# Optimization experiments

Measured on AMD Instinct MI355X. Metric: run time of the kernel, lower is better.

The kernel has to match this reference:

```python
import jax, jax.numpy as jnp
import numpy as np

EMBED = 512
MLP_DIM = 2048
B, T = 4, 4096
EPS = 1e-5


def setup_inputs() -> dict:
    key = jax.random.key(0)
    ks = jax.random.split(key, 8)
    s = lambda fan_in: 1.0 / np.sqrt(fan_in)
    inp = {
        "x": jax.random.normal(ks[0], (B, T, EMBED), dtype=jnp.float32),
        "Wq": jax.random.uniform(ks[1], (EMBED, EMBED), jnp.float32, -s(EMBED), s(EMBED)),
        "bq": jnp.zeros((EMBED,), jnp.float32),
        "Wk": jax.random.uniform(ks[2], (EMBED, EMBED), jnp.float32, -s(EMBED), s(EMBED)),
        "bk": jnp.zeros((EMBED,), jnp.float32),
        "Wv": jax.random.uniform(ks[3], (EMBED, EMBED), jnp.float32, -s(EMBED), s(EMBED)),
        "bv": jnp.zeros((EMBED,), jnp.float32),
        "W1": jax.random.uniform(ks[4], (EMBED, MLP_DIM), jnp.float32, -s(EMBED), s(EMBED)),
        "b1": jnp.zeros((MLP_DIM,), jnp.float32),
        "W2": jax.random.uniform(ks[5], (MLP_DIM, EMBED), jnp.float32, -s(MLP_DIM), s(MLP_DIM)),
        "b2": jnp.zeros((EMBED,), jnp.float32),
        "ln1_g": jnp.ones((EMBED,), jnp.float32),
        "ln1_b": jnp.zeros((EMBED,), jnp.float32),
        "ln2_g": jnp.ones((EMBED,), jnp.float32),
        "ln2_b": jnp.zeros((EMBED,), jnp.float32),
    }
    return inp


def _layernorm(x, g, b):
    mu = x.mean(-1, keepdims=True)
    var = ((x - mu) ** 2).mean(-1, keepdims=True)
    return (x - mu) * jax.lax.rsqrt(var + EPS) * g + b


def reference(x, Wq, bq, Wk, bk, Wv, bv, W1, b1, W2, b2, ln1_g, ln1_b, ln2_g, ln2_b):
    # pre-LN causal self-attention (single head)
    h = _layernorm(x, ln1_g, ln1_b)
    q = h @ Wq + bq  # [B,T,D]
    k = h @ Wk + bk
    v = h @ Wv + bv
    scale = 1.0 / jnp.sqrt(jnp.float32(EMBED))
    scores = jnp.einsum("btd,bsd->bts", q, k) * scale  # [B,T,T]
    mask = jnp.tril(jnp.ones((T, T), dtype=bool))
    scores = jnp.where(mask, scores, -jnp.inf)
    # NOTE: source applies softmax over the ENTIRE [T,T] matrix per batch
    # element (global max + global sum), not per-row. Replicate exactly.
    m = scores.max(axis=(-2, -1), keepdims=True)
    e = jnp.exp(scores - m)
    attn = e / e.sum(axis=(-2, -1), keepdims=True)
    x = x + jnp.einsum("bts,bsd->btd", attn, v)
    # MLP
    h2 = _layernorm(x, ln2_g, ln2_b)
    x = x + (jax.nn.gelu(h2 @ W1 + b1, approximate=False) @ W2 + b2)
    return x
```

## Files before the change

kernel.cpp:

```cpp
#include <hip/hip_runtime.h>
#include <hip/hip_bf16.h>
#include <math.h>

#define EMBED 512
#define MLPD  2048
#define NB    4
#define TS    4096
#define BT    (NB*TS)
#define BK    64
#define NTILES_TRI 528

typedef __attribute__((ext_vector_type(4))) float f32x4;
typedef __attribute__((ext_vector_type(8))) short s16x8;
typedef __hip_bfloat16 bf16_t;

__device__ __forceinline__ void gload16(const void* g, void* l) {
  __builtin_amdgcn_global_load_lds(
      (const __attribute__((address_space(1))) void*)g,
      (__attribute__((address_space(3))) void*)l, 16, 0, 0);
}

__device__ __forceinline__ float fast_erf(float y) {
  const float ay = fabsf(y);
  const float t = __builtin_amdgcn_rcpf(1.0f + 0.3275911f*ay);
  float poly = 1.061405429f;
  poly = poly*t - 1.453152027f;
  poly = poly*t + 1.421413741f;
  poly = poly*t - 0.284496736f;
  poly = poly*t + 0.254829592f;
  poly = poly*t;
  const float e = 1.0f - poly*__expf(-ay*ay);
  return copysignf(e, y);
}

__device__ __forceinline__ void gemm_core(
    const bf16_t* __restrict__ A, int lda,
    const bf16_t* __restrict__ Bt, int ldb,
    int kmax, bf16_t* Alds, bf16_t* Blds, f32x4 acc[4][4])
{
  const int tid = threadIdx.x;
  const int w  = tid >> 6;
  const int l  = tid & 63;
  const int wr = w >> 1, wc = w & 1;
  const int fr = l & 15, fg = l >> 4;

  #pragma unroll
  for (int i = 0; i < 4; ++i)
    #pragma unroll
    for (int j = 0; j < 4; ++j)
      #pragma unroll
      for (int e = 0; e < 4; ++e)
        acc[i][j][e] = 0.0f;

  const int srow = w*32 + (l >> 3);
  const int scol = (l & 7)*8;

  for (int k0 = 0; k0 < kmax; k0 += BK) {
    __syncthreads();
    #pragma unroll
    for (int c = 0; c < 4; ++c) {
      const bf16_t* ga = A  + (size_t)(srow + c*8)*lda + (k0 + scol);
      const bf16_t* gb = Bt + (size_t)(srow + c*8)*ldb + (k0 + scol);
      gload16(ga, Alds + (w*32 + c*8)*BK);
      gload16(gb, Blds + (w*32 + c*8)*BK);
    }
    __syncthreads();
    #pragma unroll
    for (int kk = 0; kk < BK; kk += 32) {
      s16x8 av[4], bv[4];
      #pragma unroll
      for (int mf = 0; mf < 4; ++mf)
        av[mf] = *(const s16x8*)(Alds + (wr*64 + mf*16 + fr)*BK + kk + fg*8);
      #pragma unroll
      for (int nf = 0; nf < 4; ++nf)
        bv[nf] = *(const s16x8*)(Blds + (wc*64 + nf*16 + fr)*BK + kk + fg*8);
      #pragma unroll
      for (int mf = 0; mf < 4; ++mf)
        #pragma unroll
        for (int nf = 0; nf < 4; ++nf)
          acc[mf][nf] = __builtin_amdgcn_mfma_f32_16x16x32_bf16(
              av[mf], bv[nf], acc[mf][nf], 0, 0, 0);
    }
  }
}

#define EPILOGUE_SETUP \
  const int l = threadIdx.x & 63; const int w = threadIdx.x >> 6; \
  const int wr = w >> 1, wc = w & 1, fr = l & 15, fg = l >> 4;

__global__ void __launch_bounds__(256) k_proj_qkv(
    const bf16_t* __restrict__ A,
    const bf16_t* __restrict__ wqt, const bf16_t* __restrict__ wkt,
    const bf16_t* __restrict__ wvt,
    const float* __restrict__ bq, const float* __restrict__ bk,
    const float* __restrict__ bv,
    bf16_t* __restrict__ qb, bf16_t* __restrict__ kb, bf16_t* __restrict__ vt)
{
  __shared__ __align__(16) bf16_t Alds[128*BK];
  __shared__ __align__(16) bf16_t Blds[128*BK];
  f32x4 acc[4][4];
  const int z = blockIdx.z;
  const bf16_t* Wt = (z == 0) ? wqt : (z == 1) ? wkt : wvt;
  const float* bias = (z == 0) ? bq : (z == 1) ? bk : bv;
  const int m0 = blockIdx.x*128, n0 = blockIdx.y*128;
  gemm_core(A + (size_t)m0*EMBED, EMBED, Wt + (size_t)n0*EMBED, EMBED, EMBED,
            Alds, Blds, acc);
  EPILOGUE_SETUP
  if (z < 2) {
    bf16_t* outp = (z == 0) ? qb : kb;
    #pragma unroll
    for (int mf = 0; mf < 4; ++mf)
      #pragma unroll
      for (int nf = 0; nf < 4; ++nf) {
        const int col = n0 + wc*64 + nf*16 + fr;
        const float bb = bias[col];
        #pragma unroll
        for (int j = 0; j < 4; ++j) {
          const int row = m0 + wr*64 + mf*16 + fg*4 + j;
          outp[(size_t)row*EMBED + col] = __float2bfloat16(acc[mf][nf][j] + bb);
        }
      }
  } else {
    #pragma unroll
    for (int mf = 0; mf < 4; ++mf)
      #pragma unroll
      for (int nf = 0; nf < 4; ++nf) {
        const int col = n0 + wc*64 + nf*16 + fr;
        const float bb = bias[col];
        #pragma unroll
        for (int j = 0; j < 4; ++j) {
          const int row = m0 + wr*64 + mf*16 + fg*4 + j;
          const int b = row >> 12, t = row & 4095;
          vt[((size_t)b*EMBED + col)*TS + t] = __float2bfloat16(acc[mf][nf][j] + bb);
        }
      }
  }
}

__global__ void __launch_bounds__(256) k_attn1(
    const bf16_t* __restrict__ q, const bf16_t* __restrict__ kmat,
    bf16_t* __restrict__ P, float* __restrict__ partials, int serial_b)
{
  __shared__ __align__(16) bf16_t Alds[128*BK];
  __shared__ __align__(16) bf16_t Blds[128*BK];
  int b, r;
  if (serial_b >= 0) {
    b = serial_b; r = blockIdx.x;
  } else {
    const int L = blockIdx.x;
    const int logical = (L & 7)*264 + (L >> 3);
    b = logical / NTILES_TRI;
    r = logical - b*NTILES_TRI;
  }
  int ti = (int)((sqrtf(8.0f*(float)r + 1.0f) - 1.0f)*0.5f);
  while ((ti + 1)*(ti + 2)/2 <= r) ++ti;
  while (ti*(ti + 1)/2 > r) --ti;
  const int tj = r - ti*(ti + 1)/2;

  f32x4 acc[4][4];
  const bf16_t* A  = q    + ((size_t)b*TS + (size_t)ti*128)*EMBED;
  const bf16_t* Bt = kmat + ((size_t)b*TS + (size_t)tj*128)*EMBED;
  gemm_core(A, EMBED, Bt, EMBED, EMBED, Alds, Blds, acc);

  EPILOGUE_SETUP
  bf16_t* Pb = P + (size_t)((serial_b >= 0) ? 0 : b)*TS*TS;
  const float SC = 0.044194173824159216f;
  float lsum = 0.0f;
  #pragma unroll
  for (int mf = 0; mf < 4; ++mf)
    #pragma unroll
    for (int nf = 0; nf < 4; ++nf) {
      const int gs = tj*128 + wc*64 + nf*16 + fr;
      #pragma unroll
      for (int j = 0; j < 4; ++j) {
        const int gt = ti*128 + wr*64 + mf*16 + fg*4 + j;
        float e = 0.0f;
        if (gs <= gt) e = __expf(acc[mf][nf][j]*SC - 30.0f);
        Pb[(size_t)gt*TS + gs] = __float2bfloat16(e);
        lsum += e;
      }
    }
  #pragma unroll
  for (int off = 32; off > 0; off >>= 1) lsum += __shfl_xor(lsum, off);
  __shared__ float red[4];
  if (l == 0) red[w] = lsum;
  __syncthreads();
  if (threadIdx.x == 0)
    partials[(size_t)b*NTILES_TRI + r] = red[0] + red[1] + red[2] + red[3];
}

__global__ void k_reduce(const float* __restrict__ part, float* __restrict__ S, int n)
{
  const int b = blockIdx.x;
  const int l = threadIdx.x;
  float s = 0.0f;
  for (int i = l; i < n; i += 64) s += part[(size_t)b*n + i];
  #pragma unroll
  for (int off = 32; off > 0; off >>= 1) s += __shfl_xor(s, off);
  if (l == 0) S[b] = s;
}

__global__ void __launch_bounds__(256) k_attn2(
    const bf16_t* __restrict__ P, const bf16_t* __restrict__ vt,
    const float* __restrict__ S, const float* __restrict__ x,
    float* __restrict__ out, int serial_b)
{
  __shared__ __align__(16) bf16_t Alds[128*BK];
  __shared__ __align__(16) bf16_t Blds[128*BK];
  int ti, nj, b;
  if (serial_b >= 0) {
    ti = blockIdx.x; nj = blockIdx.y; b = serial_b;
  } else {
    const int L = blockIdx.x;
    const int xc = L & 7;
    const int idx = L >> 3;
    nj = idx & 3;
    const int s = idx >> 2;
    b = s & 3;
    const int which = s >> 2;
    ti = (which == 0) ? 2*xc
       : (which == 1) ? 2*xc + 1
       : (which == 2) ? 30 - 2*xc
                      : 31 - 2*xc;
  }
  f32x4 acc[4][4];
  const bf16_t* A  = P + (size_t)((serial_b >= 0) ? 0 : b)*TS*TS + (size_t)ti*128*TS;
  const bf16_t* Bt = vt + ((size_t)b*EMBED + (size_t)nj*128)*TS;
  const int kmax = (ti + 1)*128;
  gemm_core(A, TS, Bt, TS, kmax, Alds, Blds, acc);

  EPILOGUE_SETUP
  const float invS = 1.0f / S[b];
  #pragma unroll
  for (int mf = 0; mf < 4; ++mf)
    #pragma unroll
    for (int nf = 0; nf < 4; ++nf) {
      const int d = nj*128 + wc*64 + nf*16 + fr;
      #pragma unroll
      for (int j = 0; j < 4; ++j) {
        const int t = ti*128 + wr*64 + mf*16 + fg*4 + j;
        const size_t idx2 = ((size_t)b*TS + t)*EMBED + d;
        out[idx2] = x[idx2] + acc[mf][nf][j]*invS;
      }
    }
}

__global__ void __launch_bounds__(256) k_mlp1(
    const bf16_t* __restrict__ A, const bf16_t* __restrict__ Wt,
    const float* __restrict__ bias, bf16_t* __restrict__ mid)
{
  __shared__ __align__(16) bf16_t Alds[128*BK];
  __shared__ __align__(16) bf16_t Blds[128*BK];
  f32x4 acc[4][4];
  const int m0 = blockIdx.x*128, n0 = blockIdx.y*128;
  gemm_core(A + (size_t)m0*EMBED, EMBED, Wt + (size_t)n0*EMBED, EMBED, EMBED,
            Alds, Blds, acc);
  EPILOGUE_SETUP
  #pragma unroll
  for (int mf = 0; mf < 4; ++mf)
    #pragma unroll
    for (int nf = 0; nf < 4; ++nf) {
      const int col = n0 + wc*64 + nf*16 + fr;
      const float bb = bias[col];
      #pragma unroll
      for (int j = 0; j < 4; ++j) {
        const int row = m0 + wr*64 + mf*16 + fg*4 + j;
        const float pre = acc[mf][nf][j] + bb;
        const float ge = 0.5f*pre*(1.0f + fast_erf(pre*0.70710678118654752f));
        mid[(size_t)row*MLPD + col] = __float2bfloat16(ge);
      }
    }
}

__global__ void __launch_bounds__(256) k_mlp2(
    const bf16_t* __restrict__ A, const bf16_t* __restrict__ Wt,
    const float* __restrict__ bias, float* __restrict__ out)
{
  __shared__ __align__(16) bf16_t Alds[128*BK];
  __shared__ __align__(16) bf16_t Blds[128*BK];
  f32x4 acc[4][4];
  const int m0 = blockIdx.x*128, n0 = blockIdx.y*128;
  gemm_core(A + (size_t)m0*MLPD, MLPD, Wt + (size_t)n0*MLPD, MLPD, MLPD,
            Alds, Blds, acc);
  EPILOGUE_SETUP
  #pragma unroll
  for (int mf = 0; mf < 4; ++mf)
    #pragma unroll
    for (int nf = 0; nf < 4; ++nf) {
      const int col = n0 + wc*64 + nf*16 + fr;
      const float bb = bias[col];
      #pragma unroll
      for (int j = 0; j < 4; ++j) {
        const int row = m0 + wr*64 + mf*16 + fg*4 + j;
        const size_t idx = (size_t)row*EMBED + col;
        out[idx] = out[idx] + acc[mf][nf][j] + bb;
      }
    }
}

__global__ void __launch_bounds__(256) k_ln(
    const float* __restrict__ x, const float* __restrict__ g,
    const float* __restrict__ bta, bf16_t* __restrict__ h)
{
  const int row = blockIdx.x*4 + (threadIdx.x >> 6);
  const int l = threadIdx.x & 63;
  const float4* xr = (const float4*)(x + (size_t)row*EMBED);
  const float4 a = xr[l*2], c = xr[l*2 + 1];
  float vals[8] = {a.x, a.y, a.z, a.w, c.x, c.y, c.z, c.w};
  float s = 0.0f, ss = 0.0f;
  #pragma unroll
  for (int i = 0; i < 8; ++i) { s += vals[i]; ss += vals[i]*vals[i]; }
  #pragma unroll
  for (int off = 32; off > 0; off >>= 1) {
    s  += __shfl_xor(s,  off);
    ss += __shfl_xor(ss, off);
  }
  const float mu = s*(1.0f/EMBED);
  const float var = ss*(1.0f/EMBED) - mu*mu;
  const float rs = rsqrtf(var + 1e-5f);
  const float4* g4 = (const float4*)g;
  const float4* b4 = (const float4*)bta;
  const float4 ga = g4[l*2], gc = g4[l*2 + 1];
  const float4 ba = b4[l*2], bc = b4[l*2 + 1];
  const float gv[8] = {ga.x, ga.y, ga.z, ga.w, gc.x, gc.y, gc.z, gc.w};
  const float bv[8] = {ba.x, ba.y, ba.z, ba.w, bc.x, bc.y, bc.z, bc.w};
  s16x8 ov;
  bf16_t* ovp = (bf16_t*)&ov;
  #pragma unroll
  for (int i = 0; i < 8; ++i)
    ovp[i] = __float2bfloat16((vals[i] - mu)*rs*gv[i] + bv[i]);
  *((s16x8*)(h + (size_t)row*EMBED) + l) = ov;
}

__global__ void __launch_bounds__(256) k_transpose_all(
    const float* __restrict__ Wq, const float* __restrict__ Wk,
    const float* __restrict__ Wv, const float* __restrict__ W1,
    const float* __restrict__ W2,
    bf16_t* __restrict__ wqt, bf16_t* __restrict__ wkt,
    bf16_t* __restrict__ wvt, bf16_t* __restrict__ w1t,
    bf16_t* __restrict__ w2t)
{
  __shared__ float tile[32][33];
  int L = blockIdx.x;
  const float* W; bf16_t* Wt; int Kd, Nd, t;
  if (L < 768) {
    const int m = L >> 8; t = L & 255;
    W  = (m == 0) ? Wq : (m == 1) ? Wk : Wv;
    Wt = (m == 0) ? wqt : (m == 1) ? wkt : wvt;
    Kd = EMBED; Nd = EMBED;
  } else if (L < 1792) {
    t = L - 768;  W = W1; Wt = w1t; Kd = EMBED; Nd = MLPD;
  } else {
    t = L - 1792; W = W2; Wt = w2t; Kd = MLPD; Nd = EMBED;
  }
  const int ntx = Nd >> 5;
  const int tx32 = (t % ntx)*32, ty32 = (t / ntx)*32;
  const int x = threadIdx.x & 31, y8 = threadIdx.x >> 5;
  #pragma unroll
  for (int r = 0; r < 4; ++r) {
    const int y = y8 + r*8;
    tile[y][x] = W[(size_t)(ty32 + y)*Nd + tx32 + x];
  }
  __syncthreads();
  #pragma unroll
  for (int r = 0; r < 4; ++r) {
    const int y = y8 + r*8;
    Wt[(size_t)(tx32 + y)*Kd + ty32 + x] = __float2bfloat16(tile[x][y]);
  }
}

extern "C" void kernel_launch(void* const* d_in, const int* in_sizes, int n_in,
                              void* d_out, int out_size, void* d_ws, size_t ws_size,
                              hipStream_t stream) {
  (void)in_sizes; (void)n_in; (void)out_size;
  const float* x   = (const float*)d_in[0];
  const float* Wq  = (const float*)d_in[1];
  const float* bq  = (const float*)d_in[2];
  const float* Wk  = (const float*)d_in[3];
  const float* bk  = (const float*)d_in[4];
  const float* Wv  = (const float*)d_in[5];
  const float* bv  = (const float*)d_in[6];
  const float* W1  = (const float*)d_in[7];
  const float* b1  = (const float*)d_in[8];
  const float* W2  = (const float*)d_in[9];
  const float* b2  = (const float*)d_in[10];
  const float* g1  = (const float*)d_in[11];
  const float* be1 = (const float*)d_in[12];
  const float* g2  = (const float*)d_in[13];
  const float* be2 = (const float*)d_in[14];
  float* out = (float*)d_out;

  char* p = (char*)d_ws;
  auto alloc = [&](size_t bytes) -> char* {
    char* r = p; p += (bytes + 255) & ~(size_t)255; return r;
  };
  bf16_t* h   = (bf16_t*)alloc((size_t)BT*EMBED*2);
  bf16_t* wqt = (bf16_t*)alloc((size_t)EMBED*EMBED*2);
  bf16_t* wkt = (bf16_t*)alloc((size_t)EMBED*EMBED*2);
  bf16_t* wvt = (bf16_t*)alloc((size_t)EMBED*EMBED*2);
  bf16_t* w1t = (bf16_t*)alloc((size_t)MLPD*EMBED*2);
  bf16_t* w2t = (bf16_t*)alloc((size_t)EMBED*MLPD*2);
  bf16_t* qb  = (bf16_t*)alloc((size_t)BT*EMBED*2);
  bf16_t* kb  = (bf16_t*)alloc((size_t)BT*EMBED*2);
  bf16_t* vtb = (bf16_t*)alloc((size_t)BT*EMBED*2);
  float* partials = (float*)alloc((size_t)NB*NTILES_TRI*sizeof(float));
  float* S = (float*)alloc(256);

  const size_t mid_bytes = (size_t)BT*MLPD*2;
  const size_t p_full    = (size_t)NB*TS*TS*2;
  const size_t used = (size_t)(p - (char*)d_ws);
  const bool full = ws_size >= used + (p_full > mid_bytes ? p_full : mid_bytes);
  char* region = alloc(full ? p_full : mid_bytes);
  bf16_t* P   = (bf16_t*)region;
  bf16_t* mid = (bf16_t*)region;

  k_transpose_all<<<dim3(2816), 256, 0, stream>>>(Wq, Wk, Wv, W1, W2,
                                                  wqt, wkt, wvt, w1t, w2t);
  k_ln<<<BT/4, 256, 0, stream>>>(x, g1, be1, h);

  k_proj_qkv<<<dim3(BT/128, EMBED/128, 3), 256, 0, stream>>>(
      h, wqt, wkt, wvt, bq, bk, bv, qb, kb, vtb);

  if (full) {
    k_attn1<<<dim3(NB*NTILES_TRI), 256, 0, stream>>>(qb, kb, P, partials, -1);
    k_reduce<<<NB, 64, 0, stream>>>(partials, S, NTILES_TRI);
    k_attn2<<<dim3(512), 256, 0, stream>>>(P, vtb, S, x, out, -1);
  } else {
    for (int b = 0; b < NB; ++b) {
      k_attn1<<<dim3(NTILES_TRI), 256, 0, stream>>>(qb, kb, P, partials, b);
      k_reduce<<<1, 64, 0, stream>>>(partials + (size_t)b*NTILES_TRI, S + b, NTILES_TRI);
      k_attn2<<<dim3(TS/128, EMBED/128), 256, 0, stream>>>(P, vtb, S, x, out, b);
    }
  }

  k_ln<<<BT/4, 256, 0, stream>>>(out, g2, be2, h);
  k_mlp1<<<dim3(BT/128, MLPD/128), 256, 0, stream>>>(h, w1t, b1, mid);
  k_mlp2<<<dim3(BT/128, EMBED/128), 256, 0, stream>>>(mid, w2t, b2, out);
}
```

Before: 353.4 us.

## Double-buffer LDS tiles in attention-PV and MLP2 GEMMs with async prefetch

Adds a double-buffered GEMM core that issues global-to-LDS loads for the next K tile before computing on the current one. It waits with a partial vmcnt so those loads overlap the MFMA work, and uses raw barriers in place of syncthreads. The attention PV kernel and the second MLP GEMM switch to it, which doubles their LDS use to 64KB per block and may lower occupancy. The manual waitcnt handling is fragile if the compiler reorders or adds memory ops.

```diff
diff --git a/kernel.cpp b/kernel.cpp
--- a/kernel.cpp
+++ b/kernel.cpp
@@ -81,6 +81,77 @@
           acc[mf][nf] = __builtin_amdgcn_mfma_f32_16x16x32_bf16(
               av[mf], bv[nf], acc[mf][nf], 0, 0, 0);
     }
+  }
+}
+
+__device__ __forceinline__ void gemm_core_db(
+    const bf16_t* __restrict__ A, int lda,
+    const bf16_t* __restrict__ Bt, int ldb,
+    int kmax, bf16_t* Alds, bf16_t* Blds, f32x4 acc[4][4])
+{
+  const int tid = threadIdx.x;
+  const int w  = tid >> 6;
+  const int l  = tid & 63;
+  const int wr = w >> 1, wc = w & 1;
+  const int fr = l & 15, fg = l >> 4;
+
+  #pragma unroll
+  for (int i = 0; i < 4; ++i)
+    #pragma unroll
+    for (int j = 0; j < 4; ++j)
+      #pragma unroll
+      for (int e = 0; e < 4; ++e)
+        acc[i][j][e] = 0.0f;
+
+  const int srow = w*32 + (l >> 3);
+  const int scol = (l & 7)*8;
+  const int T = kmax >> 6;
+
+  {
+    const bf16_t* ga = A  + (size_t)srow*lda + scol;
+    const bf16_t* gb = Bt + (size_t)srow*ldb + scol;
+    #pragma unroll
+    for (int c = 0; c < 4; ++c) {
+      gload16(ga + (size_t)(c*8)*lda, Alds + (w*32 + c*8)*BK);
+      gload16(gb + (size_t)(c*8)*ldb, Blds + (w*32 + c*8)*BK);
+    }
+  }
+
+  for (int t = 0; t < T; ++t) {
+    const int cur = t & 1;
+    bf16_t* Ac = Alds + cur*(128*BK);
+    bf16_t* Bc = Blds + cur*(128*BK);
+    if (t + 1 < T) {
+      const int k0 = (t + 1)*BK;
+      bf16_t* An = Alds + (cur^1)*(128*BK);
+      bf16_t* Bn = Blds + (cur^1)*(128*BK);
+      #pragma unroll
+      for (int c = 0; c < 4; ++c) {
+        gload16(A  + (size_t)(srow + c*8)*lda + (k0 + scol), An + (w*32 + c*8)*BK);
+        gload16(Bt + (size_t)(srow + c*8)*ldb + (k0 + scol), Bn + (w*32 + c*8)*BK);
+      }
+      asm volatile("s_waitcnt vmcnt(8)" ::: "memory");
+    } else {
+      asm volatile("s_waitcnt vmcnt(0)" ::: "memory");
+    }
+    __builtin_amdgcn_s_barrier();
+    #pragma unroll
+    for (int kk = 0; kk < BK; kk += 32) {
+      s16x8 av[4], bv[4];
+      #pragma unroll
+      for (int mf = 0; mf < 4; ++mf)
+        av[mf] = *(const s16x8*)(Ac + (wr*64 + mf*16 + fr)*BK + kk + fg*8);
+      #pragma unroll
+      for (int nf = 0; nf < 4; ++nf)
+        bv[nf] = *(const s16x8*)(Bc + (wc*64 + nf*16 + fr)*BK + kk + fg*8);
+      #pragma unroll
+      for (int mf = 0; mf < 4; ++mf)
+        #pragma unroll
+        for (int nf = 0; nf < 4; ++nf)
+          acc[mf][nf] = __builtin_amdgcn_mfma_f32_16x16x32_bf16(
+              av[mf], bv[nf], acc[mf][nf], 0, 0, 0);
+    }
+    __builtin_amdgcn_s_barrier();
   }
 }
 
@@ -205,8 +276,8 @@
     const float* __restrict__ S, const float* __restrict__ x,
     float* __restrict__ out, int serial_b)
 {
-  __shared__ __align__(16) bf16_t Alds[128*BK];
-  __shared__ __align__(16) bf16_t Blds[128*BK];
+  __shared__ __align__(16) bf16_t Alds[2*128*BK];
+  __shared__ __align__(16) bf16_t Blds[2*128*BK];
   int ti, nj, b;
   if (serial_b >= 0) {
     ti = blockIdx.x; nj = blockIdx.y; b = serial_b;
@@ -227,7 +298,7 @@
   const bf16_t* A  = P + (size_t)((serial_b >= 0) ? 0 : b)*TS*TS + (size_t)ti*128*TS;
   const bf16_t* Bt = vt + ((size_t)b*EMBED + (size_t)nj*128)*TS;
   const int kmax = (ti + 1)*128;
-  gemm_core(A, TS, Bt, TS, kmax, Alds, Blds, acc);
+  gemm_core_db(A, TS, Bt, TS, kmax, Alds, Blds, acc);
 
   EPILOGUE_SETUP
   const float invS = 1.0f / S[b];
@@ -276,12 +347,12 @@
     const bf16_t* __restrict__ A, const bf16_t* __restrict__ Wt,
     const float* __restrict__ bias, float* __restrict__ out)
 {
-  __shared__ __align__(16) bf16_t Alds[128*BK];
-  __shared__ __align__(16) bf16_t Blds[128*BK];
+  __shared__ __align__(16) bf16_t Alds[2*128*BK];
+  __shared__ __align__(16) bf16_t Blds[2*128*BK];
   f32x4 acc[4][4];
   const int m0 = blockIdx.x*128, n0 = blockIdx.y*128;
-  gemm_core(A + (size_t)m0*MLPD, MLPD, Wt + (size_t)n0*MLPD, MLPD, MLPD,
-            Alds, Blds, acc);
+  gemm_core_db(A + (size_t)m0*MLPD, MLPD, Wt + (size_t)n0*MLPD, MLPD, MLPD,
+               Alds, Blds, acc);
   EPILOGUE_SETUP
   #pragma unroll
   for (int mf = 0; mf < 4; ++mf)
```

Result: no change. 352.2 us (-0.3%).
